# Kernel tuning notes

Measured on AMD Instinct MI355X. Metric: run time of the kernel, lower is better.

Reference implementation:

```python
import jax, jax.numpy as jnp
import numpy as np

B, S, H, E, I = 2, 1024, 1024, 8, 512
EPS = 1e-8  # torch F.cosine_similarity eps


def setup_inputs() -> dict:
    key = jax.random.key(0)
    ks = jax.random.split(key, 5)
    return {
        "hidden_states": jax.random.normal(ks[0], (B, S, H), dtype=jnp.float32),
        "expert_embeddings": jax.random.normal(ks[1], (E, H), dtype=jnp.float32),
        # torch init is zeros; -0.03 keeps the zero-selection fallback (which NaNs the
        # original's softmax) from ever triggering while preserving ~half-dense routing
        "gate_threshold": jnp.full((E,), -0.03, dtype=jnp.float32),
        "w_gate": jax.random.normal(ks[2], (E, H, I), dtype=jnp.float32) / np.sqrt(H).astype(np.float32),
        "w_up": jax.random.normal(ks[3], (E, H, I), dtype=jnp.float32) / np.sqrt(H).astype(np.float32),
        "w_down": jax.random.normal(ks[4], (E, I, H), dtype=jnp.float32) / np.sqrt(I).astype(np.float32),
    }


def _forward(hidden_states, expert_embeddings, gate_threshold, w_gate, w_up, w_down):
    b, s, h = hidden_states.shape
    n_experts = expert_embeddings.shape[0]
    x = hidden_states.reshape(-1, h)  # [T, H]

    # cosine-similarity routing scores [T, E]
    xn = x / jnp.maximum(jnp.linalg.norm(x, axis=-1, keepdims=True), EPS)
    en = expert_embeddings / jnp.maximum(jnp.linalg.norm(expert_embeddings, axis=-1, keepdims=True), EPS)
    scores = xn @ en.T

    # SiLUHardThreshold forward: hard 0/1 mask (used only as a boolean downstream,
    # so no gradient flows through it in the module's output path)
    routing_mask = (jax.nn.silu(scores - gate_threshold) > 0).astype(scores.dtype)

    # guarantee at least one expert per token: fall back to top-1 score
    num_sel = routing_mask.sum(axis=-1)  # [T]
    top1 = jnp.argmax(scores, axis=-1)   # [T]
    routing_mask_final = jnp.where((num_sel == 0)[:, None],
                                   jax.nn.one_hot(top1, n_experts, dtype=scores.dtype),
                                   routing_mask)

    # softmax over selected experts (pre-fallback mask, as in the original)
    masked_scores = jnp.where(routing_mask > 0, scores, -jnp.inf)
    routing_weights = jax.nn.softmax(masked_scores.astype(jnp.float32), axis=-1).astype(x.dtype)
    gates = routing_weights * routing_mask_final  # [T, E] combine weights

    # per-expert Qwen3 SwiGLU MLP: down(silu(gate(x)) * up(x)); dense over experts,
    # gated combine is the vectorized equivalent of the gather/MLP/index_add loop
    hmid = jax.nn.silu(jnp.einsum('th,ehi->eti', x, w_gate)) * jnp.einsum('th,ehi->eti', x, w_up)  # [E,T,I]
    out = jnp.einsum('eti,eih,te->th', hmid, w_down, gates)  # [T, H]

    return out.reshape(b, s, h), scores


def reference(hidden_states, expert_embeddings, gate_threshold, w_gate, w_up, w_down):
    # returns (final_hidden_states [B,S,H], router_logits [T,E])
    return _forward(hidden_states, expert_embeddings, gate_threshold, w_gate, w_up, w_down)
```

## Files before the change

### kernel.cpp

```cpp
#include <hip/hip_runtime.h>
#include <hip/hip_bf16.h>
#include <stdint.h>

#define T_TOK 2048
#define H_DIM 1024
#define E_NUM 8
#define I_DIM 512
#define KDOWN (E_NUM * I_DIM)
#define EPSR 1e-8f

typedef short s16x8 __attribute__((ext_vector_type(8)));
typedef float f32x4 __attribute__((ext_vector_type(4)));

static __device__ __forceinline__ uint16_t f2bf(float f) {
    union { float f; uint32_t i; } v; v.f = f;
    uint32_t lsb = (v.i >> 16) & 1u;
    v.i += 0x7fffu + lsb;
    return (uint16_t)(v.i >> 16);
}

static __device__ __forceinline__ void gll16(const void* g, void* l) {
    __builtin_amdgcn_global_load_lds(
        (const __attribute__((address_space(1))) void*)g,
        (__attribute__((address_space(3))) void*)l, 16, 0, 0);
}

__global__ __launch_bounds__(256) void prep_kernel(
    const float* __restrict__ wg, const float* __restrict__ wu,
    const float* __restrict__ wd, uint16_t* __restrict__ wgT,
    uint16_t* __restrict__ wuT, uint16_t* __restrict__ wdT,
    const float* __restrict__ x, const float* __restrict__ emb,
    const float* __restrict__ thr, float* __restrict__ scores_out,
    float* __restrict__ gates, uint16_t* __restrict__ xb) {
    __shared__ union {
        float tile[64][68];
        struct { float semb[E_NUM * H_DIM]; float senorm[E_NUM]; } r;
    } sm;
    const int bid = blockIdx.x;
    const int tid = threadIdx.x;

    if (bid < 3072) {
        const int bz = bid >> 7, by = (bid >> 3) & 15, bx = bid & 7;
        const float* src; uint16_t* dst; int C, out_stride, r0, c0;
        if (bz < 16) {
            const int e = bz & 7;
            src = (bz < 8 ? wg : wu) + (long)e * H_DIM * I_DIM;
            dst = (bz < 8 ? wgT : wuT) + (long)e * I_DIM * H_DIM;
            C = I_DIM; out_stride = H_DIM;
            r0 = by * 64; c0 = bx * 64;
        } else {
            const int e = bz - 16;
            src = wd + (long)e * I_DIM * H_DIM;
            dst = wdT + (long)e * I_DIM;
            C = H_DIM; out_stride = KDOWN;
            r0 = bx * 64; c0 = by * 64;
        }
        const int g16 = tid >> 4, l16 = (tid & 15) * 4;
        #pragma unroll
        for (int it = 0; it < 4; ++it) {
            int r = it * 16 + g16;
            *(float4*)&sm.tile[r][l16] = *(const float4*)(src + (long)(r0 + r) * C + c0 + l16);
        }
        __syncthreads();
        #pragma unroll
        for (int it = 0; it < 4; ++it) {
            int oc = it * 16 + g16;
            ushort4 o;
            o.x = f2bf(sm.tile[l16 + 0][oc]);
            o.y = f2bf(sm.tile[l16 + 1][oc]);
            o.z = f2bf(sm.tile[l16 + 2][oc]);
            o.w = f2bf(sm.tile[l16 + 3][oc]);
            *(ushort4*)(dst + (long)(c0 + oc) * out_stride + r0 + l16) = o;
        }
        return;
    }
    const int rb = bid - 3072;
    const int lane = tid & 63;
    const int wave = tid >> 6;
    for (int i = tid; i < E_NUM * H_DIM; i += 256) sm.r.semb[i] = emb[i];
    __syncthreads();
    for (int e = wave; e < E_NUM; e += 4) {
        float s = 0.f;
        #pragma unroll
        for (int c = 0; c < 16; ++c) { float v = sm.r.semb[e * H_DIM + lane + 64 * c]; s += v * v; }
        #pragma unroll
        for (int off = 32; off; off >>= 1) s += __shfl_xor(s, off);
        if (lane == 0) sm.r.senorm[e] = fmaxf(sqrtf(s), EPSR);
    }
    __syncthreads();
    const int t = rb * 4 + wave;
    const float* xt = x + (long)t * H_DIM;
    uint16_t* xbt = xb + (long)t * H_DIM;
    float nrm = 0.f, dot[E_NUM];
    #pragma unroll
    for (int e = 0; e < E_NUM; ++e) dot[e] = 0.f;
    #pragma unroll
    for (int c = 0; c < 16; ++c) {
        float v = xt[lane + 64 * c];
        xbt[lane + 64 * c] = f2bf(v);
        nrm += v * v;
        #pragma unroll
        for (int e = 0; e < E_NUM; ++e) dot[e] += v * sm.r.semb[e * H_DIM + lane + 64 * c];
    }
    #pragma unroll
    for (int off = 32; off; off >>= 1) {
        nrm += __shfl_xor(nrm, off);
        #pragma unroll
        for (int e = 0; e < E_NUM; ++e) dot[e] += __shfl_xor(dot[e], off);
    }
    float xn = fmaxf(sqrtf(nrm), EPSR);
    float sc[E_NUM], sel[E_NUM];
    float msel = -1e30f, mall = -1e30f;
    int nsel = 0, arg = 0;
    #pragma unroll
    for (int e = 0; e < E_NUM; ++e) {
        sc[e] = dot[e] / (xn * sm.r.senorm[e]);
        float d = sc[e] - thr[e];
        sel[e] = (d > 0.f) ? 1.f : 0.f;
        if (d > 0.f) { nsel++; msel = fmaxf(msel, sc[e]); }
        if (sc[e] > mall) { mall = sc[e]; arg = e; }
    }
    float w[E_NUM], den = 0.f;
    #pragma unroll
    for (int e = 0; e < E_NUM; ++e) { w[e] = (sel[e] > 0.f) ? __expf(sc[e] - msel) : 0.f; den += w[e]; }
    if (lane == 0) {
        #pragma unroll
        for (int e = 0; e < E_NUM; ++e) {
            scores_out[t * E_NUM + e] = sc[e];
            gates[t * E_NUM + e] = (nsel > 0) ? (w[e] / den) : ((e == arg) ? 1.f : 0.f);
        }
    }
}

__global__ __launch_bounds__(256, 2) void moe_gateup_kernel(
    const uint16_t* __restrict__ xb,
    const uint16_t* __restrict__ wgT,
    const uint16_t* __restrict__ wuT,
    const float* __restrict__ gates,
    uint16_t* __restrict__ hmid) {
    const int bid = blockIdx.x + 16 * (blockIdx.y + 4 * blockIdx.z);
    const int e  = bid & 7;
    const int j  = bid >> 3;
    const int t0 = (j & 15) * 128;
    const int i0 = (j >> 4) * 128;
    __shared__ uint16_t sA[128][64];
    __shared__ uint16_t sG[128][64];
    __shared__ uint16_t sU[128][64];
    __shared__ float sGate[128];
    const int tid  = threadIdx.x;
    const int lane = tid & 63;
    const int wave = tid >> 6;
    const int wm = wave >> 1, wn = wave & 1;
    if (tid < 128) sGate[tid] = gates[(t0 + tid) * E_NUM + e];

    const int srow = wave * 32 + (lane >> 3);
    const int scol = ((lane & 7) ^ (srow & 7)) * 8;
    const uint16_t* ga = xb  + (long)(t0 + srow) * H_DIM + scol;
    const uint16_t* gg = wgT + ((long)e * I_DIM + i0 + srow) * H_DIM + scol;
    const uint16_t* gu = wuT + ((long)e * I_DIM + i0 + srow) * H_DIM + scol;

    f32x4 accg[4][4] = {}, accu[4][4] = {};
    const int q = lane >> 4, r16 = lane & 15;
    const int sw = r16 & 7;

    for (int kb = 0; kb < H_DIM; kb += 64) {
        __syncthreads();
        #pragma unroll
        for (int j2 = 0; j2 < 4; ++j2) {
            const int lr = wave * 32 + j2 * 8;
            gll16(ga + (long)j2 * 8 * H_DIM + kb, &sA[lr][0]);
            gll16(gg + (long)j2 * 8 * H_DIM + kb, &sG[lr][0]);
            gll16(gu + (long)j2 * 8 * H_DIM + kb, &sU[lr][0]);
        }
        __syncthreads();
        #pragma unroll
        for (int kk = 0; kk < 2; ++kk) {
            const int pc = ((kk * 4 + q) ^ sw) * 8;
            s16x8 af[4], gf[4], uf[4];
            #pragma unroll
            for (int m = 0; m < 4; ++m)
                af[m] = *(const s16x8*)&sA[wm * 64 + m * 16 + r16][pc];
            #pragma unroll
            for (int n = 0; n < 4; ++n) {
                gf[n] = *(const s16x8*)&sG[wn * 64 + n * 16 + r16][pc];
                uf[n] = *(const s16x8*)&sU[wn * 64 + n * 16 + r16][pc];
            }
            #pragma unroll
            for (int m = 0; m < 4; ++m)
                #pragma unroll
                for (int n = 0; n < 4; ++n) {
                    accg[m][n] = __builtin_amdgcn_mfma_f32_16x16x32_bf16(af[m], gf[n], accg[m][n], 0, 0, 0);
                    accu[m][n] = __builtin_amdgcn_mfma_f32_16x16x32_bf16(af[m], uf[n], accu[m][n], 0, 0, 0);
                }
        }
    }
    #pragma unroll
    for (int m = 0; m < 4; ++m) {
        #pragma unroll
        for (int rr = 0; rr < 4; ++rr) {
            const int trow = wm * 64 + m * 16 + q * 4 + rr;
            const float gate = sGate[trow];
            const long base = (long)(t0 + trow) * KDOWN + e * I_DIM + i0;
            #pragma unroll
            for (int n = 0; n < 4; ++n) {
                float g = accg[m][n][rr], u = accu[m][n][rr];
                float h = gate * (g / (1.f + __expf(-g))) * u;
                hmid[base + wn * 64 + n * 16 + r16] = f2bf(h);
            }
        }
    }
}

__global__ __launch_bounds__(256, 3) void moe_down_kernel(
    const uint16_t* __restrict__ hmid,
    const uint16_t* __restrict__ wdT,
    float* __restrict__ out,
    float* __restrict__ parts) {
    const int bid = blockIdx.x + 8 * (blockIdx.y + 16 * blockIdx.z);
    const int r  = bid & 7;
    const int j  = bid >> 3;
    const int h0 = ((r & 1) * 4 + (j & 3)) * 128;
    const int t0 = ((r >> 1) * 4 + ((j >> 2) & 3)) * 128;
    const int kz = j >> 4;
    const int kst = kz * 1024;
    __shared__ uint16_t sA[128][64];
    __shared__ uint16_t sB[128][64];
    const int tid  = threadIdx.x;
    const int lane = tid & 63;
    const int wave = tid >> 6;
    const int wm = wave >> 1, wn = wave & 1;

    const int srow = wave * 32 + (lane >> 3);
    const int scol = ((lane & 7) ^ (srow & 7)) * 8;
    const uint16_t* ga = hmid + (long)(t0 + srow) * KDOWN + scol;
    const uint16_t* gb = wdT  + (long)(h0 + srow) * KDOWN + scol;

    f32x4 acc[4][4] = {};
    const int q = lane >> 4, r16 = lane & 15;
    const int sw = r16 & 7;

    for (int kb = kst; kb < kst + 1024; kb += 64) {
        __syncthreads();
        #pragma unroll
        for (int j2 = 0; j2 < 4; ++j2) {
            const int lr = wave * 32 + j2 * 8;
            gll16(ga + (long)j2 * 8 * KDOWN + kb, &sA[lr][0]);
            gll16(gb + (long)j2 * 8 * KDOWN + kb, &sB[lr][0]);
        }
        __syncthreads();
        #pragma unroll
        for (int kk = 0; kk < 2; ++kk) {
            const int pc = ((kk * 4 + q) ^ sw) * 8;
            s16x8 af[4], bf[4];
            #pragma unroll
            for (int m = 0; m < 4; ++m)
                af[m] = *(const s16x8*)&sA[wm * 64 + m * 16 + r16][pc];
            #pragma unroll
            for (int n = 0; n < 4; ++n)
                bf[n] = *(const s16x8*)&sB[wn * 64 + n * 16 + r16][pc];
            #pragma unroll
            for (int m = 0; m < 4; ++m)
                #pragma unroll
                for (int n = 0; n < 4; ++n)
                    acc[m][n] = __builtin_amdgcn_mfma_f32_16x16x32_bf16(af[m], bf[n], acc[m][n], 0, 0, 0);
        }
    }
    float* dst = (kz == 0) ? out : (parts + (long)(kz - 1) * T_TOK * H_DIM);
    #pragma unroll
    for (int m = 0; m < 4; ++m) {
        #pragma unroll
        for (int rr = 0; rr < 4; ++rr) {
            const int t = t0 + wm * 64 + m * 16 + q * 4 + rr;
            #pragma unroll
            for (int n = 0; n < 4; ++n)
                dst[(long)t * H_DIM + h0 + wn * 64 + n * 16 + r16] = acc[m][n][rr];
        }
    }
}

__global__ __launch_bounds__(256) void reduce_kernel(float* __restrict__ out,
                                                     const float* __restrict__ parts) {
    long i = ((long)blockIdx.x * 256 + threadIdx.x) * 4;
    float4 a = *(const float4*)(out + i);
    #pragma unroll
    for (int j = 0; j < 3; ++j) {
        float4 b = *(const float4*)(parts + (long)j * T_TOK * H_DIM + i);
        a.x += b.x; a.y += b.y; a.z += b.z; a.w += b.w;
    }
    *(float4*)(out + i) = a;
}

extern "C" void kernel_launch(void* const* d_in, const int* in_sizes, int n_in,
                              void* d_out, int out_size, void* d_ws, size_t ws_size,
                              hipStream_t stream) {
    const float* x    = (const float*)d_in[0];
    const float* emb  = (const float*)d_in[1];
    const float* thr  = (const float*)d_in[2];
    const float* wg   = (const float*)d_in[3];
    const float* wu   = (const float*)d_in[4];
    const float* wd   = (const float*)d_in[5];
    float* out    = (float*)d_out;
    float* scores = out + (size_t)T_TOK * H_DIM;

    uint8_t* ws = (uint8_t*)d_ws;
    uint16_t* xb   = (uint16_t*)(ws);
    uint16_t* wgT  = (uint16_t*)(ws + (size_t)4  * 1048576);
    uint16_t* wuT  = (uint16_t*)(ws + (size_t)12 * 1048576);
    uint16_t* wdT  = (uint16_t*)(ws + (size_t)20 * 1048576);
    uint16_t* hmid = (uint16_t*)(ws + (size_t)28 * 1048576);
    float*    gates = (float*)  (ws + (size_t)44 * 1048576);
    float*    parts = (float*)  (ws + (size_t)48 * 1048576);

    prep_kernel<<<3072 + T_TOK / 4, 256, 0, stream>>>(
        wg, wu, wd, wgT, wuT, wdT, x, emb, thr, scores, gates, xb);
    moe_gateup_kernel<<<dim3(T_TOK / 128, I_DIM / 128, E_NUM), 256, 0, stream>>>(
        xb, wgT, wuT, gates, hmid);
    moe_down_kernel<<<dim3(H_DIM / 128, T_TOK / 128, 4), 256, 0, stream>>>(hmid, wdT, out, parts);
    reduce_kernel<<<(T_TOK * H_DIM) / 1024, 256, 0, stream>>>(out, parts);
}
```

Baseline: 170.8 us.

## Double-buffer LDS tiles with K=32 stages in gate-up and down GEMMs

```diff
diff --git a/kernel.cpp b/kernel.cpp
--- a/kernel.cpp
+++ b/kernel.cpp
@@ -143,9 +143,9 @@
     const int j  = bid >> 3;
     const int t0 = (j & 15) * 128;
     const int i0 = (j >> 4) * 128;
-    __shared__ uint16_t sA[128][64];
-    __shared__ uint16_t sG[128][64];
-    __shared__ uint16_t sU[128][64];
+    __shared__ uint16_t sA[2][128][32];
+    __shared__ uint16_t sG[2][128][32];
+    __shared__ uint16_t sU[2][128][32];
     __shared__ float sGate[128];
     const int tid  = threadIdx.x;
     const int lane = tid & 63;
@@ -153,47 +153,51 @@
     const int wm = wave >> 1, wn = wave & 1;
     if (tid < 128) sGate[tid] = gates[(t0 + tid) * E_NUM + e];
 
-    const int srow = wave * 32 + (lane >> 3);
-    const int scol = ((lane & 7) ^ (srow & 7)) * 8;
-    const uint16_t* ga = xb  + (long)(t0 + srow) * H_DIM + scol;
-    const uint16_t* gg = wgT + ((long)e * I_DIM + i0 + srow) * H_DIM + scol;
-    const uint16_t* gu = wuT + ((long)e * I_DIM + i0 + srow) * H_DIM + scol;
+    const int lr4 = lane >> 2;
+    const int sc4 = ((lane & 3) ^ ((lane >> 3) & 3)) * 8;
+    const uint16_t* ga = xb  + (long)(t0 + wave * 32 + lr4) * H_DIM + sc4;
+    const uint16_t* gg = wgT + ((long)e * I_DIM + i0 + wave * 32 + lr4) * H_DIM + sc4;
+    const uint16_t* gu = wuT + ((long)e * I_DIM + i0 + wave * 32 + lr4) * H_DIM + sc4;
 
     f32x4 accg[4][4] = {}, accu[4][4] = {};
     const int q = lane >> 4, r16 = lane & 15;
-    const int sw = r16 & 7;
-
-    for (int kb = 0; kb < H_DIM; kb += 64) {
-        __syncthreads();
-        #pragma unroll
-        for (int j2 = 0; j2 < 4; ++j2) {
-            const int lr = wave * 32 + j2 * 8;
-            gll16(ga + (long)j2 * 8 * H_DIM + kb, &sA[lr][0]);
-            gll16(gg + (long)j2 * 8 * H_DIM + kb, &sG[lr][0]);
-            gll16(gu + (long)j2 * 8 * H_DIM + kb, &sU[lr][0]);
-        }
-        __syncthreads();
-        #pragma unroll
-        for (int kk = 0; kk < 2; ++kk) {
-            const int pc = ((kk * 4 + q) ^ sw) * 8;
-            s16x8 af[4], gf[4], uf[4];
-            #pragma unroll
-            for (int m = 0; m < 4; ++m)
-                af[m] = *(const s16x8*)&sA[wm * 64 + m * 16 + r16][pc];
+    const int pc = (q ^ ((r16 >> 1) & 3)) * 8;
+
+#define STAGE_GU(b, kb_) do {                                              \
+        _Pragma("unroll")                                                  \
+        for (int j2 = 0; j2 < 2; ++j2) {                                   \
+            const int r0s = wave * 32 + j2 * 16;                           \
+            gll16(ga + (long)(j2 * 16) * H_DIM + (kb_), &sA[b][r0s][0]);   \
+            gll16(gg + (long)(j2 * 16) * H_DIM + (kb_), &sG[b][r0s][0]);   \
+            gll16(gu + (long)(j2 * 16) * H_DIM + (kb_), &sU[b][r0s][0]);   \
+        } } while (0)
+
+    STAGE_GU(0, 0);
+    __syncthreads();
+    int cur = 0;
+    for (int t = 0; t < 32; ++t) {
+        const int kb = t * 32;
+        if (t < 31) STAGE_GU(cur ^ 1, kb + 32);
+        s16x8 af[4], gf[4], uf[4];
+        #pragma unroll
+        for (int m = 0; m < 4; ++m)
+            af[m] = *(const s16x8*)&sA[cur][wm * 64 + m * 16 + r16][pc];
+        #pragma unroll
+        for (int n = 0; n < 4; ++n) {
+            gf[n] = *(const s16x8*)&sG[cur][wn * 64 + n * 16 + r16][pc];
+            uf[n] = *(const s16x8*)&sU[cur][wn * 64 + n * 16 + r16][pc];
+        }
+        #pragma unroll
+        for (int m = 0; m < 4; ++m)
             #pragma unroll
             for (int n = 0; n < 4; ++n) {
-                gf[n] = *(const s16x8*)&sG[wn * 64 + n * 16 + r16][pc];
-                uf[n] = *(const s16x8*)&sU[wn * 64 + n * 16 + r16][pc];
+                accg[m][n] = __builtin_amdgcn_mfma_f32_16x16x32_bf16(af[m], gf[n], accg[m][n], 0, 0, 0);
+                accu[m][n] = __builtin_amdgcn_mfma_f32_16x16x32_bf16(af[m], uf[n], accu[m][n], 0, 0, 0);
             }
-            #pragma unroll
-            for (int m = 0; m < 4; ++m)
-                #pragma unroll
-                for (int n = 0; n < 4; ++n) {
-                    accg[m][n] = __builtin_amdgcn_mfma_f32_16x16x32_bf16(af[m], gf[n], accg[m][n], 0, 0, 0);
-                    accu[m][n] = __builtin_amdgcn_mfma_f32_16x16x32_bf16(af[m], uf[n], accu[m][n], 0, 0, 0);
-                }
-        }
-    }
+        __syncthreads();
+        cur ^= 1;
+    }
+#undef STAGE_GU
     #pragma unroll
     for (int m = 0; m < 4; ++m) {
         #pragma unroll
@@ -223,48 +227,52 @@
     const int t0 = ((r >> 1) * 4 + ((j >> 2) & 3)) * 128;
     const int kz = j >> 4;
     const int kst = kz * 1024;
-    __shared__ uint16_t sA[128][64];
-    __shared__ uint16_t sB[128][64];
+    __shared__ uint16_t sA[2][128][32];
+    __shared__ uint16_t sB[2][128][32];
     const int tid  = threadIdx.x;
     const int lane = tid & 63;
     const int wave = tid >> 6;
     const int wm = wave >> 1, wn = wave & 1;
 
-    const int srow = wave * 32 + (lane >> 3);
-    const int scol = ((lane & 7) ^ (srow & 7)) * 8;
-    const uint16_t* ga = hmid + (long)(t0 + srow) * KDOWN + scol;
-    const uint16_t* gb = wdT  + (long)(h0 + srow) * KDOWN + scol;
+    const int lr4 = lane >> 2;
+    const int sc4 = ((lane & 3) ^ ((lane >> 3) & 3)) * 8;
+    const uint16_t* ga = hmid + (long)(t0 + wave * 32 + lr4) * KDOWN + sc4;
+    const uint16_t* gb = wdT  + (long)(h0 + wave * 32 + lr4) * KDOWN + sc4;
 
     f32x4 acc[4][4] = {};
     const int q = lane >> 4, r16 = lane & 15;
-    const int sw = r16 & 7;
-
-    for (int kb = kst; kb < kst + 1024; kb += 64) {
-        __syncthreads();
-        #pragma unroll
-        for (int j2 = 0; j2 < 4; ++j2) {
-            const int lr = wave * 32 + j2 * 8;
-            gll16(ga + (long)j2 * 8 * KDOWN + kb, &sA[lr][0]);
-            gll16(gb + (long)j2 * 8 * KDOWN + kb, &sB[lr][0]);
-        }
-        __syncthreads();
-        #pragma unroll
-        for (int kk = 0; kk < 2; ++kk) {
-            const int pc = ((kk * 4 + q) ^ sw) * 8;
-            s16x8 af[4], bf[4];
-            #pragma unroll
-            for (int m = 0; m < 4; ++m)
-                af[m] = *(const s16x8*)&sA[wm * 64 + m * 16 + r16][pc];
+    const int pc = (q ^ ((r16 >> 1) & 3)) * 8;
+
+#define STAGE_D(b, kb_) do {                                               \
+        _Pragma("unroll")                                                  \
+        for (int j2 = 0; j2 < 2; ++j2) {                                   \
+            const int r0s = wave * 32 + j2 * 16;                           \
+            gll16(ga + (long)(j2 * 16) * KDOWN + (kb_), &sA[b][r0s][0]);   \
+            gll16(gb + (long)(j2 * 16) * KDOWN + (kb_), &sB[b][r0s][0]);   \
+        } } while (0)
+
+    STAGE_D(0, kst);
+    __syncthreads();
+    int cur = 0;
+    for (int t = 0; t < 32; ++t) {
+        const int kb = kst + t * 32;
+        if (t < 31) STAGE_D(cur ^ 1, kb + 32);
+        s16x8 af[4], bf[4];
+        #pragma unroll
+        for (int m = 0; m < 4; ++m)
+            af[m] = *(const s16x8*)&sA[cur][wm * 64 + m * 16 + r16][pc];
+        #pragma unroll
+        for (int n = 0; n < 4; ++n)
+            bf[n] = *(const s16x8*)&sB[cur][wn * 64 + n * 16 + r16][pc];
+        #pragma unroll
+        for (int m = 0; m < 4; ++m)
             #pragma unroll
             for (int n = 0; n < 4; ++n)
-                bf[n] = *(const s16x8*)&sB[wn * 64 + n * 16 + r16][pc];
-            #pragma unroll
-            for (int m = 0; m < 4; ++m)
-                #pragma unroll
-                for (int n = 0; n < 4; ++n)
-                    acc[m][n] = __builtin_amdgcn_mfma_f32_16x16x32_bf16(af[m], bf[n], acc[m][n], 0, 0, 0);
-        }
-    }
+                acc[m][n] = __builtin_amdgcn_mfma_f32_16x16x32_bf16(af[m], bf[n], acc[m][n], 0, 0, 0);
+        __syncthreads();
+        cur ^= 1;
+    }
+#undef STAGE_D
     float* dst = (kz == 0) ? out : (parts + (long)(kz - 1) * T_TOK * H_DIM);
     #pragma unroll
     for (int m = 0; m < 4; ++m) {
```

After: 191.7 us. 1.12x slower.

## Interleave gate/up weights and pipeline gate-up GEMM with 4-stage LDS buffering

Applied to the files above, without the earlier changes.

```diff
diff --git a/kernel.cpp b/kernel.cpp
--- a/kernel.cpp
+++ b/kernel.cpp
@@ -27,8 +27,8 @@
 
 __global__ __launch_bounds__(256) void prep_kernel(
     const float* __restrict__ wg, const float* __restrict__ wu,
-    const float* __restrict__ wd, uint16_t* __restrict__ wgT,
-    uint16_t* __restrict__ wuT, uint16_t* __restrict__ wdT,
+    const float* __restrict__ wd, uint16_t* __restrict__ wB,
+    uint16_t* __restrict__ wdT,
     const float* __restrict__ x, const float* __restrict__ emb,
     const float* __restrict__ thr, float* __restrict__ scores_out,
     float* __restrict__ gates, uint16_t* __restrict__ xb) {
@@ -41,36 +41,51 @@
 
     if (bid < 3072) {
         const int bz = bid >> 7, by = (bid >> 3) & 15, bx = bid & 7;
-        const float* src; uint16_t* dst; int C, out_stride, r0, c0;
+        const int g16 = tid >> 4, l16 = (tid & 15) * 4;
         if (bz < 16) {
             const int e = bz & 7;
-            src = (bz < 8 ? wg : wu) + (long)e * H_DIM * I_DIM;
-            dst = (bz < 8 ? wgT : wuT) + (long)e * I_DIM * H_DIM;
-            C = I_DIM; out_stride = H_DIM;
-            r0 = by * 64; c0 = bx * 64;
+            const int isU = (bz >= 8);
+            const float* src = (isU ? wu : wg) + (long)e * H_DIM * I_DIM;
+            const int r0 = by * 64, c0 = bx * 64;
+            #pragma unroll
+            for (int it = 0; it < 4; ++it) {
+                int r = it * 16 + g16;
+                *(float4*)&sm.tile[r][l16] = *(const float4*)(src + (long)(r0 + r) * I_DIM + c0 + l16);
+            }
+            __syncthreads();
+            #pragma unroll
+            for (int it = 0; it < 4; ++it) {
+                int oc = it * 16 + g16;
+                int i = c0 + oc;
+                ushort4 o;
+                o.x = f2bf(sm.tile[l16 + 0][oc]);
+                o.y = f2bf(sm.tile[l16 + 1][oc]);
+                o.z = f2bf(sm.tile[l16 + 2][oc]);
+                o.w = f2bf(sm.tile[l16 + 3][oc]);
+                long rbig = ((long)e << 10) + ((i >> 4) << 5) + (isU << 4) + (i & 15);
+                *(ushort4*)(wB + rbig * H_DIM + r0 + l16) = o;
+            }
         } else {
             const int e = bz - 16;
-            src = wd + (long)e * I_DIM * H_DIM;
-            dst = wdT + (long)e * I_DIM;
-            C = H_DIM; out_stride = KDOWN;
-            r0 = bx * 64; c0 = by * 64;
-        }
-        const int g16 = tid >> 4, l16 = (tid & 15) * 4;
-        #pragma unroll
-        for (int it = 0; it < 4; ++it) {
-            int r = it * 16 + g16;
-            *(float4*)&sm.tile[r][l16] = *(const float4*)(src + (long)(r0 + r) * C + c0 + l16);
-        }
-        __syncthreads();
-        #pragma unroll
-        for (int it = 0; it < 4; ++it) {
-            int oc = it * 16 + g16;
-            ushort4 o;
-            o.x = f2bf(sm.tile[l16 + 0][oc]);
-            o.y = f2bf(sm.tile[l16 + 1][oc]);
-            o.z = f2bf(sm.tile[l16 + 2][oc]);
-            o.w = f2bf(sm.tile[l16 + 3][oc]);
-            *(ushort4*)(dst + (long)(c0 + oc) * out_stride + r0 + l16) = o;
+            const float* src = wd + (long)e * I_DIM * H_DIM;
+            uint16_t* dst = wdT + (long)e * I_DIM;
+            const int r0 = bx * 64, c0 = by * 64;
+            #pragma unroll
+            for (int it = 0; it < 4; ++it) {
+                int r = it * 16 + g16;
+                *(float4*)&sm.tile[r][l16] = *(const float4*)(src + (long)(r0 + r) * H_DIM + c0 + l16);
+            }
+            __syncthreads();
+            #pragma unroll
+            for (int it = 0; it < 4; ++it) {
+                int oc = it * 16 + g16;
+                ushort4 o;
+                o.x = f2bf(sm.tile[l16 + 0][oc]);
+                o.y = f2bf(sm.tile[l16 + 1][oc]);
+                o.z = f2bf(sm.tile[l16 + 2][oc]);
+                o.w = f2bf(sm.tile[l16 + 3][oc]);
+                *(ushort4*)(dst + (long)(c0 + oc) * KDOWN + r0 + l16) = o;
+            }
         }
         return;
     }
@@ -132,80 +147,114 @@
     }
 }
 
-__global__ __launch_bounds__(256, 2) void moe_gateup_kernel(
+__global__ __launch_bounds__(512, 2) void moe_gateup_kernel(
     const uint16_t* __restrict__ xb,
-    const uint16_t* __restrict__ wgT,
-    const uint16_t* __restrict__ wuT,
+    const uint16_t* __restrict__ wB,
     const float* __restrict__ gates,
     uint16_t* __restrict__ hmid) {
-    const int bid = blockIdx.x + 16 * (blockIdx.y + 4 * blockIdx.z);
-    const int e  = bid & 7;
-    const int j  = bid >> 3;
-    const int t0 = (j & 15) * 128;
-    const int i0 = (j >> 4) * 128;
-    __shared__ uint16_t sA[128][64];
-    __shared__ uint16_t sG[128][64];
-    __shared__ uint16_t sU[128][64];
-    __shared__ float sGate[128];
+    const int bid = blockIdx.x;
+    const int xcd = bid & 7, j = bid >> 3;
+    const int by = xcd * 4 + (j >> 3);
+    const int bx = j & 7;
+    const int t0 = bx * 256;
+    const int n0 = by * 256;
+    const int e  = by >> 2;
+
+    __shared__ uint16_t sA[4][256][32];
+    __shared__ uint16_t sB[4][256][32];
+    __shared__ float sGate[256];
+
     const int tid  = threadIdx.x;
     const int lane = tid & 63;
     const int wave = tid >> 6;
-    const int wm = wave >> 1, wn = wave & 1;
-    if (tid < 128) sGate[tid] = gates[(t0 + tid) * E_NUM + e];
-
-    const int srow = wave * 32 + (lane >> 3);
-    const int scol = ((lane & 7) ^ (srow & 7)) * 8;
-    const uint16_t* ga = xb  + (long)(t0 + srow) * H_DIM + scol;
-    const uint16_t* gg = wgT + ((long)e * I_DIM + i0 + srow) * H_DIM + scol;
-    const uint16_t* gu = wuT + ((long)e * I_DIM + i0 + srow) * H_DIM + scol;
-
-    f32x4 accg[4][4] = {}, accu[4][4] = {};
+    const int wm = wave >> 2, wn = wave & 3;
+
+    if (tid < 256) sGate[tid] = gates[(t0 + tid) * E_NUM + e];
+    __syncthreads();
+
+    const int lr = lane >> 2;
+    const int cl = ((lane & 3) ^ ((lane >> 3) & 3)) * 8;
+    const uint16_t* gA = xb + (long)(t0 + wave * 16 + lr) * H_DIM + cl;
+    const uint16_t* gB = wB + (long)(n0 + wave * 16 + lr) * H_DIM + cl;
+
+#define STA(sl, kt) do { \
+        gll16(gA + (long)(kt) * 32,                &sA[sl][wave * 16][0]); \
+        gll16(gA + 128L * H_DIM + (long)(kt) * 32, &sA[sl][128 + wave * 16][0]); } while (0)
+#define STB(sl, kt) do { \
+        gll16(gB + (long)(kt) * 32,                &sB[sl][wave * 16][0]); \
+        gll16(gB + 128L * H_DIM + (long)(kt) * 32, &sB[sl][128 + wave * 16][0]); } while (0)
+
     const int q = lane >> 4, r16 = lane & 15;
-    const int sw = r16 & 7;
-
-    for (int kb = 0; kb < H_DIM; kb += 64) {
-        __syncthreads();
-        #pragma unroll
-        for (int j2 = 0; j2 < 4; ++j2) {
-            const int lr = wave * 32 + j2 * 8;
-            gll16(ga + (long)j2 * 8 * H_DIM + kb, &sA[lr][0]);
-            gll16(gg + (long)j2 * 8 * H_DIM + kb, &sG[lr][0]);
-            gll16(gu + (long)j2 * 8 * H_DIM + kb, &sU[lr][0]);
-        }
-        __syncthreads();
-        #pragma unroll
-        for (int kk = 0; kk < 2; ++kk) {
-            const int pc = ((kk * 4 + q) ^ sw) * 8;
-            s16x8 af[4], gf[4], uf[4];
-            #pragma unroll
-            for (int m = 0; m < 4; ++m)
-                af[m] = *(const s16x8*)&sA[wm * 64 + m * 16 + r16][pc];
-            #pragma unroll
-            for (int n = 0; n < 4; ++n) {
-                gf[n] = *(const s16x8*)&sG[wn * 64 + n * 16 + r16][pc];
-                uf[n] = *(const s16x8*)&sU[wn * 64 + n * 16 + r16][pc];
-            }
-            #pragma unroll
-            for (int m = 0; m < 4; ++m)
-                #pragma unroll
-                for (int n = 0; n < 4; ++n) {
-                    accg[m][n] = __builtin_amdgcn_mfma_f32_16x16x32_bf16(af[m], gf[n], accg[m][n], 0, 0, 0);
-                    accu[m][n] = __builtin_amdgcn_mfma_f32_16x16x32_bf16(af[m], uf[n], accu[m][n], 0, 0, 0);
-                }
-        }
-    }
-    #pragma unroll
-    for (int m = 0; m < 4; ++m) {
+    const int pc = (q ^ ((r16 >> 1) & 3)) * 8;
+
+    f32x4 acc[8][4] = {};
+
+    STA(0, 0); STB(0, 0);
+    STA(1, 1); STB(1, 1);
+    STA(2, 2); STB(2, 2);
+    asm volatile("s_waitcnt vmcnt(8)" ::: "memory");
+    __builtin_amdgcn_s_barrier();
+    asm volatile("" ::: "memory");
+
+    #pragma unroll 1
+    for (int s = 0; s < 32; ++s) {
+        const int sl = s & 3;
+        s16x8 af[8], bf[4];
+        #pragma unroll
+        for (int m = 0; m < 8; ++m)
+            af[m] = *(const s16x8*)&sA[sl][wm * 128 + m * 16 + r16][pc];
+        bf[0] = *(const s16x8*)&sB[sl][wn * 64 + 0 * 16 + r16][pc];
+        bf[1] = *(const s16x8*)&sB[sl][wn * 64 + 1 * 16 + r16][pc];
+        if (s + 3 < 32) STA((s + 3) & 3, s + 3);
+        asm volatile("" ::: "memory");
+        __builtin_amdgcn_s_barrier();
+        asm volatile("" ::: "memory");
+        __builtin_amdgcn_s_setprio(1);
+        #pragma unroll
+        for (int m = 0; m < 8; ++m) {
+            acc[m][0] = __builtin_amdgcn_mfma_f32_16x16x32_bf16(af[m], bf[0], acc[m][0], 0, 0, 0);
+            acc[m][1] = __builtin_amdgcn_mfma_f32_16x16x32_bf16(af[m], bf[1], acc[m][1], 0, 0, 0);
+        }
+        __builtin_amdgcn_s_setprio(0);
+        asm volatile("" ::: "memory");
+        __builtin_amdgcn_s_barrier();
+        asm volatile("" ::: "memory");
+        bf[2] = *(const s16x8*)&sB[sl][wn * 64 + 2 * 16 + r16][pc];
+        bf[3] = *(const s16x8*)&sB[sl][wn * 64 + 3 * 16 + r16][pc];
+        if (s + 3 < 32) STB((s + 3) & 3, s + 3);
+        if (s < 29)      asm volatile("s_waitcnt vmcnt(8)" ::: "memory");
+        else if (s == 29) asm volatile("s_waitcnt vmcnt(4)" ::: "memory");
+        else             asm volatile("s_waitcnt vmcnt(0)" ::: "memory");
+        __builtin_amdgcn_s_barrier();
+        asm volatile("" ::: "memory");
+        __builtin_amdgcn_s_setprio(1);
+        #pragma unroll
+        for (int m = 0; m < 8; ++m) {
+            acc[m][2] = __builtin_amdgcn_mfma_f32_16x16x32_bf16(af[m], bf[2], acc[m][2], 0, 0, 0);
+            acc[m][3] = __builtin_amdgcn_mfma_f32_16x16x32_bf16(af[m], bf[3], acc[m][3], 0, 0, 0);
+        }
+        __builtin_amdgcn_s_setprio(0);
+        asm volatile("" ::: "memory");
+        __builtin_amdgcn_s_barrier();
+        asm volatile("" ::: "memory");
+    }
+#undef STA
+#undef STB
+
+    #pragma unroll
+    for (int m = 0; m < 8; ++m) {
         #pragma unroll
         for (int rr = 0; rr < 4; ++rr) {
-            const int trow = wm * 64 + m * 16 + q * 4 + rr;
+            const int trow = wm * 128 + m * 16 + q * 4 + rr;
             const float gate = sGate[trow];
-            const long base = (long)(t0 + trow) * KDOWN + e * I_DIM + i0;
-            #pragma unroll
-            for (int n = 0; n < 4; ++n) {
-                float g = accg[m][n][rr], u = accu[m][n][rr];
+            const long tglob = t0 + trow;
+            #pragma unroll
+            for (int p = 0; p < 2; ++p) {
+                float g = acc[m][2 * p][rr], u = acc[m][2 * p + 1][rr];
                 float h = gate * (g / (1.f + __expf(-g))) * u;
-                hmid[base + wn * 64 + n * 16 + r16] = f2bf(h);
+                const int cb = n0 + wn * 64 + p * 32;
+                const int i = (((cb & 1023) >> 5) << 4) + r16;
+                hmid[tglob * KDOWN + e * I_DIM + i] = f2bf(h);
             }
         }
     }
@@ -304,17 +353,15 @@
 
     uint8_t* ws = (uint8_t*)d_ws;
     uint16_t* xb   = (uint16_t*)(ws);
-    uint16_t* wgT  = (uint16_t*)(ws + (size_t)4  * 1048576);
-    uint16_t* wuT  = (uint16_t*)(ws + (size_t)12 * 1048576);
+    uint16_t* wB   = (uint16_t*)(ws + (size_t)4  * 1048576);
     uint16_t* wdT  = (uint16_t*)(ws + (size_t)20 * 1048576);
     uint16_t* hmid = (uint16_t*)(ws + (size_t)28 * 1048576);
     float*    gates = (float*)  (ws + (size_t)44 * 1048576);
     float*    parts = (float*)  (ws + (size_t)48 * 1048576);
 
     prep_kernel<<<3072 + T_TOK / 4, 256, 0, stream>>>(
-        wg, wu, wd, wgT, wuT, wdT, x, emb, thr, scores, gates, xb);
-    moe_gateup_kernel<<<dim3(T_TOK / 128, I_DIM / 128, E_NUM), 256, 0, stream>>>(
-        xb, wgT, wuT, gates, hmid);
+        wg, wu, wd, wB, wdT, x, emb, thr, scores, gates, xb);
+    moe_gateup_kernel<<<256, 512, 0, stream>>>(xb, wB, gates, hmid);
     moe_down_kernel<<<dim3(H_DIM / 128, T_TOK / 128, 4), 256, 0, stream>>>(hmid, wdT, out, parts);
     reduce_kernel<<<(T_TOK * H_DIM) / 1024, 256, 0, stream>>>(out, parts);
 }
```

Result: no change. 173.5 us (median of 2 runs) (+1.6%).
